# Kernel optimization log

Hardware: AMD Instinct MI355X
Metric: run time of the kernel (lower is better)

## Reference

```python
import jax, jax.numpy as jnp
from jax import lax
import numpy as np

N_ENT = 50000
N_REL = 500
E = 800000
H = 128
BS = 1024
C = 96
KER = 7
KH, KW = 8, 16  # H = KH*KW
TOPK = 15
FLAT = C * (2 * KH - KER + 1) * (KW - KER + 1)  # 96*10*10 = 9600


def mlp3(x, w0, b0, w1, b1, w2, b2):
    x = jax.nn.relu(x @ w0 + b0)
    x = jax.nn.relu(x @ w1 + b1)
    return x @ w2 + b2


def compute_corr(x1, x2):
    x1 = x1 - jnp.mean(x1, 0, keepdims=True)
    x2 = x2 - jnp.mean(x2, 0, keepdims=True)
    s1 = jnp.sqrt(jnp.mean(x1 * x1))
    s2 = jnp.sqrt(jnp.mean(x2 * x2))
    return jnp.abs(jnp.mean(x1 * x2)) / (s1 * s2)


def comp_layer(node_emb, rel_emb, src, dst, rel_id, neigh_w):
    # CompGCN 'mul' composition: u_mul_e
    comp = node_emb[src] * rel_emb[rel_id]                      # (E,H)
    score = jnp.sum(comp * node_emb[dst], axis=-1)              # e_dot_v, (E,)
    # edge softmax over incoming edges of each dst node
    m = jax.ops.segment_max(score, dst, num_segments=N_ENT)
    e = jnp.exp(score - m[dst])
    z = jax.ops.segment_sum(e, dst, num_segments=N_ENT)
    norm = e / z[dst]                                           # (E,)
    # select_topk: keep top-15 in-edges per dst by norm
    order = jnp.lexsort((-norm, dst))                           # sort by dst, then norm desc
    deg = jax.ops.segment_sum(jnp.ones((E,), jnp.int32), dst, num_segments=N_ENT)
    start = jnp.cumsum(deg) - deg                               # group start per node
    rank = jnp.arange(E, dtype=jnp.int32) - start[dst[order]]
    keep = jnp.zeros((E,), bool).at[order].set(rank < TOPK)
    w = norm * keep                                             # weighted, pruned
    # copy_e + sum aggregation to dst
    neigh = jax.ops.segment_sum(comp * w[:, None], dst, num_segments=N_ENT)
    return jnp.tanh(neigh @ neigh_w)


def conve(head, rel, ent_emb, conv_w, conv_b, fc_w, fc_b, score_b):
    x = jnp.concatenate([head.reshape(-1, 1, KH, KW), rel.reshape(-1, 1, KH, KW)], axis=2)  # (bs,1,16,16)
    x = lax.conv_general_dilated(x, conv_w, (1, 1), 'VALID') + conv_b[None, :, None, None]
    x = jax.nn.relu(x).reshape(x.shape[0], -1)                  # (bs,FLAT)
    x = jax.nn.relu(x @ fc_w + fc_b)                            # (bs,H)
    return jax.nn.sigmoid(x @ ent_emb.T + score_b)              # (bs,N_ENT)


def setup_inputs() -> dict:
    key = jax.random.key(0)
    ks = jax.random.split(key, 24)
    def g(i, shape, scale=0.05):
        return jax.random.normal(ks[i], shape, jnp.float32) * scale
    return dict(
        h_id=jax.random.randint(ks[0], (BS,), 0, N_ENT),
        r_id=jax.random.randint(ks[1], (BS,), 0, 2 * N_REL),
        src=jax.random.randint(ks[2], (E,), 0, N_ENT),
        dst=jax.random.randint(ks[3], (E,), 0, N_ENT),
        rel_id=jax.random.randint(ks[4], (E,), 0, 2 * N_REL),
        ent_emb=g(5, (N_ENT, H)),
        rel_emb0=g(6, (2 * N_REL, H)),
        neigh_w=g(7, (H, H)),
        S_w=g(8, (H, H)), S_b=jnp.zeros((H,), jnp.float32),
        L_w=g(9, (H, H)), L_b=jnp.zeros((H,), jnp.float32),
        pred_rel_emb=g(10, (2 * N_REL, H)),
        phi_w0=g(11, (H, 200)), phi_b0=jnp.zeros((200,), jnp.float32),
        phi_w1=g(12, (200, 200)), phi_b1=jnp.zeros((200,), jnp.float32),
        phi_w2=g(13, (200, 1)), phi_b2=jnp.zeros((1,), jnp.float32),
        psi_w0=g(14, (H, 200)), psi_b0=jnp.zeros((200,), jnp.float32),
        psi_w1=g(15, (200, 200)), psi_b1=jnp.zeros((200,), jnp.float32),
        psi_w2=g(16, (200, 1)), psi_b2=jnp.zeros((1,), jnp.float32),
        conv_w=g(17, (C, 1, KER, KER)), conv_b=jnp.zeros((C,), jnp.float32),
        fc_w=g(18, (FLAT, H)), fc_b=jnp.zeros((H,), jnp.float32),
        score_b=jnp.zeros((N_ENT,), jnp.float32),
    )


def reference(h_id, r_id, src, dst, rel_id,
              ent_emb, rel_emb0, neigh_w, S_w, S_b, L_w, L_b, pred_rel_emb,
              phi_w0, phi_b0, phi_w1, phi_b1, phi_w2, phi_b2,
              psi_w0, psi_b0, psi_w1, psi_b1, psi_w2, psi_b2,
              conv_w, conv_b, fc_w, fc_b, score_b):
    common = ent_emb @ S_w + S_b
    private = ent_emb @ L_w + L_b
    c1 = comp_layer(common, rel_emb0, src, dst, rel_id, neigh_w)
    c2 = comp_layer(private, rel_emb0, src, dst, rel_id, neigh_w)
    ent_out = ent_emb + c1 + c2
    corr = compute_corr(mlp3(c1, phi_w0, phi_b0, phi_w1, phi_b1, phi_w2, phi_b2),
                        mlp3(c2, psi_w0, psi_b0, psi_w1, psi_b1, psi_w2, psi_b2))
    head = ent_out[h_id]
    rel = pred_rel_emb[r_id]
    score = conve(head, rel, ent_out, conv_w, conv_b, fc_w, fc_b, score_b)
    return (score, corr)
```

## Files before the change

kernel.cpp:

```cpp
#include <hip/hip_runtime.h>
#include <math.h>

typedef unsigned short ushort;
typedef unsigned int   uint;
typedef unsigned char  uchar;
typedef short bf16x8 __attribute__((ext_vector_type(8)));
typedef float f32x4  __attribute__((ext_vector_type(4)));
typedef float f32x2  __attribute__((ext_vector_type(2)));
typedef ushort u16x8 __attribute__((ext_vector_type(8)));
typedef ushort u16x4 __attribute__((ext_vector_type(4)));

#define N_ENTS   50000
#define E_EDGES  800000
#define HD       128
#define BSZ      1024
#define C_CH     96
#define FLATD    9600
#define TOPK_K   15
#define HIDD     200
#define SPLITK   10
#define OUT_SCORE ((size_t)BSZ * N_ENTS)

#define MPAD     50048
#define NPAD_ENT 50176
#define KPAD200  224
#define NPAD200  256
#define L2E      1.4426950408889634f

#define OFF_EP       ((size_t)0)
#define OFF_ENTOUT   ((size_t)25624576)
#define OFF_RELBF    ((size_t)38469632)
#define OFF_PRELBF   ((size_t)38725632)
#define OFF_SWT      ((size_t)38981632)
#define OFF_LWT      ((size_t)39014400)
#define OFF_NWT      ((size_t)39047168)
#define OFF_P0T      ((size_t)39079936)
#define OFF_Q0T      ((size_t)39145472)
#define OFF_P1T      ((size_t)39211008)
#define OFF_Q1T      ((size_t)39325696)
#define OFF_FCT      ((size_t)39440384)
#define OFF_SC       ((size_t)41897984)
#define OFF_W        ((size_t)48297984)
#define OFF_SIDX     ((size_t)54697984)
#define OFF_DEG      ((size_t)70697984)
#define OFF_START    ((size_t)70897984)
#define OFF_CUR      ((size_t)71097984)
#define OFF_BSUM     ((size_t)71297984)
#define OFF_X1       ((size_t)71302080)
#define OFF_X2       ((size_t)71502080)
#define OFF_XFC      ((size_t)71702336)
#define OFF_ARENA    ((size_t)71964480)
#define OFF_EPQ      ((size_t)116807488)

__device__ inline ushort f2b(float f) {
    uint u = __float_as_uint(f);
    return (ushort)((u + 0x7fffu + ((u >> 16) & 1u)) >> 16);
}
__device__ inline float b2f(ushort u) { return __uint_as_float((uint)u << 16); }
__device__ inline float fexp2(float x) { return __builtin_amdgcn_exp2f(x); }
__device__ inline float frcp(float x)  { return __builtin_amdgcn_rcpf(x); }
__device__ inline float fsigmoid(float x) { return frcp(1.f + fexp2(-x * L2E)); }
__device__ inline float ftanh(float x) {
    float ax = fabsf(x);
    float t = fexp2(ax * (-2.f * L2E));
    float r = (1.f - t) * frcp(1.f + t);
    return copysignf(r, x);
}

__device__ inline uchar enc8(float x) {
    x *= 16.f;
    uint s = (__float_as_uint(x) >> 24) & 0x80u;
    float ax = fabsf(x);
    if (ax < 0.0009765625f) return (uchar)s;
    if (ax < 0.015625f) {
        int m = (int)roundf(ax * 512.f);
        if (m > 7) return (uchar)(s | 0x08);
        return (uchar)(s | m);
    }
    int ee; float fr = frexpf(ax, &ee);
    int e = ee + 6;
    int m = (int)roundf((fr * 2.f - 1.f) * 8.f);
    if (m == 8) { m = 0; e += 1; }
    if (e > 15) { e = 15; m = 6; }
    return (uchar)(s | (e << 3) | m);
}
__device__ inline float dec8s(uchar b) {
    uint e = (b >> 3) & 15u, m = b & 7u;
    float v = e ? __uint_as_float(((e + 120u) << 23) | (m << 20))
                : (float)m * 0.001953125f;
    return (b & 0x80u) ? -v : v;
}
template <int WORD>
__device__ inline f32x2 d8pk(uint u) {
#if __has_builtin(__builtin_amdgcn_cvt_pk_f32_fp8)
    return __builtin_amdgcn_cvt_pk_f32_fp8(u, WORD);
#else
    uint h = WORD ? (u >> 16) : u;
    f32x2 r;
    r.x = dec8s((uchar)(h & 0xffu));
    r.y = dec8s((uchar)((h >> 8) & 0xffu));
    return r;
#endif
}

__global__ void k_cvt(const float* __restrict__ in, ushort* __restrict__ out,
                      int M, int Mpad, int K) {
    int i = blockIdx.x * 256 + threadIdx.x;
    if (i >= Mpad * K) return;
    int r = i / K;
    out[i] = (r < M) ? f2b(in[i]) : (ushort)0;
}

__global__ void k_cvt2(const float* __restrict__ in0, ushort* __restrict__ out0,
                       const float* __restrict__ in1, ushort* __restrict__ out1, int n) {
    const float* in = blockIdx.z ? in1 : in0;
    ushort* out = blockIdx.z ? out1 : out0;
    int i = blockIdx.x * 256 + threadIdx.x;
    if (i < n) out[i] = f2b(in[i]);
}

__global__ __launch_bounds__(256) void k_tcvtT(const float* __restrict__ in, ushort* __restrict__ out,
                                               int K, int N, int Kpad, int Npad) {
    __shared__ float t[32][33];
    int k0 = blockIdx.x * 32, n0 = blockIdx.y * 32;
    int tx = threadIdx.x & 31, ty = threadIdx.x >> 5;
    for (int i = ty; i < 32; i += 8) {
        int k = k0 + i, n = n0 + tx;
        t[i][tx] = (k < K && n < N) ? in[(size_t)k * N + n] : 0.f;
    }
    __syncthreads();
    for (int i = ty; i < 32; i += 8) {
        int n = n0 + i, k = k0 + tx;
        if (n < Npad && k < Kpad) out[(size_t)n * Kpad + k] = f2b(t[tx][i]);
    }
}

__global__ __launch_bounds__(256) void k_tcvt7(
    const float* __restrict__ S_w, const float* __restrict__ L_w, const float* __restrict__ n_w,
    const float* __restrict__ p0, const float* __restrict__ q0,
    const float* __restrict__ p1, const float* __restrict__ q1,
    ushort* __restrict__ Swt, ushort* __restrict__ Lwt, ushort* __restrict__ nWt,
    ushort* __restrict__ p0t, ushort* __restrict__ q0t,
    ushort* __restrict__ p1t, ushort* __restrict__ q1t) {
    const float* in; ushort* out; int K, N, Kp, Np;
    switch (blockIdx.z) {
        case 0: in = S_w; out = Swt; K = 128; N = 128; Kp = 128; Np = 128; break;
        case 1: in = L_w; out = Lwt; K = 128; N = 128; Kp = 128; Np = 128; break;
        case 2: in = n_w; out = nWt; K = 128; N = 128; Kp = 128; Np = 128; break;
        case 3: in = p0;  out = p0t; K = 128; N = HIDD; Kp = 128; Np = NPAD200; break;
        case 4: in = q0;  out = q0t; K = 128; N = HIDD; Kp = 128; Np = NPAD200; break;
        case 5: in = p1;  out = p1t; K = HIDD; N = HIDD; Kp = KPAD200; Np = NPAD200; break;
        default: in = q1; out = q1t; K = HIDD; N = HIDD; Kp = KPAD200; Np = NPAD200; break;
    }
    __shared__ float t[32][33];
    int k0 = blockIdx.x * 32, n0 = blockIdx.y * 32;
    if (k0 >= Kp || n0 >= Np) return;
    int tx = threadIdx.x & 31, ty = threadIdx.x >> 5;
    for (int i = ty; i < 32; i += 8) {
        int k = k0 + i, n = n0 + tx;
        t[i][tx] = (k < K && n < N) ? in[(size_t)k * N + n] : 0.f;
    }
    __syncthreads();
    for (int i = ty; i < 32; i += 8) {
        int n = n0 + i, k = k0 + tx;
        if (n < Np && k < Kp) out[(size_t)n * Kp + k] = f2b(t[tx][i]);
    }
}

template <int WM, int WN, int OUTBF, int FUSE2>
__global__ __launch_bounds__(256) void k_mgemm(
    const ushort* __restrict__ A, int lda,
    const ushort* __restrict__ Bt, int ldb,
    const float* __restrict__ bias, void* __restrict__ Cout, int ldc,
    int M, int N, int K, int kChunk, int epi, int iofs, int npad,
    const ushort* __restrict__ A2, const ushort* __restrict__ Bt2,
    const float* __restrict__ bias2, void* __restrict__ Cout2, int iofs2,
    uchar* __restrict__ q8) {
    if (FUSE2 && blockIdx.z == 1) { A = A2; Bt = Bt2; bias = bias2; Cout = Cout2; iofs = iofs2; }
    const int w = threadIdx.x >> 6, lane = threadIdx.x & 63;
    const int wr = w / WN, wc = w % WN;
    const int row0 = blockIdx.x * (WM * 64) + wr * 64;
    const int col0 = blockIdx.y * (WN * 64) + wc * 64;
    const int lr = lane & 15;
    const int kg = (lane >> 4) * 8;
    const int kb = FUSE2 ? 0 : blockIdx.z * kChunk;
    const int ke = kb + kChunk;

    f32x4 acc[4][4];
#pragma unroll
    for (int i = 0; i < 4; i++)
#pragma unroll
        for (int j = 0; j < 4; j++) acc[i][j] = (f32x4){0.f, 0.f, 0.f, 0.f};

    for (int kk = kb; kk < ke; kk += 32) {
        bf16x8 af[4], bfr[4];
#pragma unroll
        for (int i = 0; i < 4; i++) {
            int r = row0 + i * 16 + lr;
            r = min(r, M - 1);
            af[i] = *(const bf16x8*)(A + (size_t)r * lda + kk + kg);
        }
#pragma unroll
        for (int j = 0; j < 4; j++) {
            int c = col0 + j * 16 + lr;
            bfr[j] = *(const bf16x8*)(Bt + (size_t)c * ldb + kk + kg);
        }
#pragma unroll
        for (int i = 0; i < 4; i++)
#pragma unroll
            for (int j = 0; j < 4; j++)
                acc[i][j] = __builtin_amdgcn_mfma_f32_16x16x32_bf16(af[i], bfr[j], acc[i][j], 0, 0, 0);
    }

    const int cr = (lane >> 4) * 4, cc = lane & 15;
    if (!FUSE2 && gridDim.z > 1) {
        float* P = (float*)Cout + (size_t)blockIdx.z * M * ldc;
#pragma unroll
        for (int i = 0; i < 4; i++)
#pragma unroll
            for (int j = 0; j < 4; j++) {
                int col = col0 + j * 16 + cc;
                if (col >= N) continue;
#pragma unroll
                for (int t = 0; t < 4; t++) {
                    int row = row0 + i * 16 + cr + t;
                    if (row < M) P[(size_t)row * ldc + col] = acc[i][j][t];
                }
            }
    } else {
#pragma unroll
        for (int i = 0; i < 4; i++)
#pragma unroll
            for (int j = 0; j < 4; j++) {
                int col = col0 + j * 16 + cc;
                if (col >= (OUTBF ? npad : N)) continue;
                bool valid = col < N;
                float bi = (bias && valid) ? bias[col] : 0.f;
#pragma unroll
                for (int t = 0; t < 4; t++) {
                    int row = row0 + i * 16 + cr + t;
                    if (row >= M) continue;
                    float v = acc[i][j][t] + bi;
                    if (epi == 1) v = fmaxf(v, 0.f);
                    else if (epi == 2) v = ftanh(v);
                    else if (epi == 3) v = fsigmoid(v);
                    if (!valid) v = 0.f;
                    if (OUTBF) {
                        size_t idx = (iofs < 0) ? ((size_t)row * ldc + col)
                                   : ((size_t)row * ldc + ((size_t)(col >> 1) << 2) + (col & 1) + iofs);
                        ((ushort*)Cout)[idx] = f2b(v);
                        if (q8 && iofs >= 0) q8[idx] = enc8(v);
                    } else {
                        ((float*)Cout)[(size_t)row * ldc + col] = v;
                    }
                }
            }
    }
}

__global__ __launch_bounds__(256) void k_tanh2ent(
    const ushort* __restrict__ neigh1, const ushort* __restrict__ neigh2,
    const ushort* __restrict__ nWt, const float* __restrict__ ent,
    ushort* __restrict__ c1o, ushort* __restrict__ c2o, ushort* __restrict__ eo) {
    const int w = threadIdx.x >> 6, lane = threadIdx.x & 63;
    const int wr = w >> 1, wc = w & 1;
    const int row0 = blockIdx.x * 128 + wr * 64;
    const int col0 = wc * 64;
    const int lr = lane & 15, kg = (lane >> 4) * 8;

    f32x4 a1[4][4], a2[4][4];
#pragma unroll
    for (int i = 0; i < 4; i++)
#pragma unroll
        for (int j = 0; j < 4; j++) { a1[i][j] = (f32x4){0,0,0,0}; a2[i][j] = (f32x4){0,0,0,0}; }

    for (int kk = 0; kk < HD; kk += 32) {
        bf16x8 f1[4], f2v[4], bfr[4];
#pragma unroll
        for (int i = 0; i < 4; i++) {
            int r = min(row0 + i * 16 + lr, N_ENTS - 1);
            f1[i]  = *(const bf16x8*)(neigh1 + (size_t)r * HD + kk + kg);
            f2v[i] = *(const bf16x8*)(neigh2 + (size_t)r * HD + kk + kg);
        }
#pragma unroll
        for (int j = 0; j < 4; j++)
            bfr[j] = *(const bf16x8*)(nWt + (size_t)(col0 + j * 16 + lr) * HD + kk + kg);
#pragma unroll
        for (int i = 0; i < 4; i++)
#pragma unroll
            for (int j = 0; j < 4; j++) {
                a1[i][j] = __builtin_amdgcn_mfma_f32_16x16x32_bf16(f1[i],  bfr[j], a1[i][j], 0, 0, 0);
                a2[i][j] = __builtin_amdgcn_mfma_f32_16x16x32_bf16(f2v[i], bfr[j], a2[i][j], 0, 0, 0);
            }
    }

    const int cr = (lane >> 4) * 4, cc = lane & 15;
#pragma unroll
    for (int i = 0; i < 4; i++)
#pragma unroll
        for (int j = 0; j < 4; j++) {
            int col = col0 + j * 16 + cc;
#pragma unroll
            for (int t = 0; t < 4; t++) {
                int row = row0 + i * 16 + cr + t;
                if (row >= N_ENTS) continue;
                float t1 = ftanh(a1[i][j][t]);
                float t2 = ftanh(a2[i][j][t]);
                size_t idx = (size_t)row * HD + col;
                c1o[idx] = f2b(t1);
                c2o[idx] = f2b(t2);
                eo[idx] = f2b(ent[idx] + t1 + t2);
            }
        }
}

__global__ __launch_bounds__(256) void k_score(
    const ushort* __restrict__ A, const ushort* __restrict__ Bt,
    const float* __restrict__ bias, float* __restrict__ C, int N) {
    __shared__ __align__(16) float st[4][16][68];
    const int w = threadIdx.x >> 6, lane = threadIdx.x & 63;
    const int lr = lane & 15, kg = (lane >> 4) * 8;
    const int cr = (lane >> 4) * 4, cc = lane & 15;
    int flat = blockIdx.y * 16 + blockIdx.x;
    int swz = (flat & 7) * 392 + (flat >> 3);
    const int row0 = (swz & 15) * 64;
    const int colw = (swz >> 4) * 256 + w * 64;

    f32x4 acc[4][4];
#pragma unroll
    for (int i = 0; i < 4; i++)
#pragma unroll
        for (int j = 0; j < 4; j++) acc[i][j] = (f32x4){0.f, 0.f, 0.f, 0.f};

    for (int kk = 0; kk < HD; kk += 32) {
        bf16x8 af[4], bfr[4];
#pragma unroll
        for (int i = 0; i < 4; i++)
            af[i] = *(const bf16x8*)(A + (size_t)(row0 + i * 16 + lr) * HD + kk + kg);
#pragma unroll
        for (int j = 0; j < 4; j++)
            bfr[j] = *(const bf16x8*)(Bt + (size_t)(colw + j * 16 + lr) * HD + kk + kg);
#pragma unroll
        for (int i = 0; i < 4; i++)
#pragma unroll
            for (int j = 0; j < 4; j++)
                acc[i][j] = __builtin_amdgcn_mfma_f32_16x16x32_bf16(af[i], bfr[j], acc[i][j], 0, 0, 0);
    }

#pragma unroll
    for (int i = 0; i < 4; i++) {
#pragma unroll
        for (int j = 0; j < 4; j++) {
            int col = colw + j * 16 + cc;
            float bi = (col < N) ? bias[col] : 0.f;
#pragma unroll
            for (int t = 0; t < 4; t++)
                st[w][cr + t][j * 16 + cc] = fsigmoid(acc[i][j][t] + bi);
        }
#pragma unroll
        for (int p = 0; p < 4; p++) {
            int r = p * 4 + (lane >> 4);
            int cq = (lane & 15) * 4;
            f32x4 v = *(const f32x4*)&st[w][r][cq];
            int gc = colw + cq;
            if (gc < N)
                __builtin_nontemporal_store(v, (f32x4*)&C[(size_t)(row0 + i * 16 + r) * N + gc]);
        }
    }
}

__global__ __launch_bounds__(256) void k_mlp2(
    const ushort* __restrict__ A0, const ushort* __restrict__ W0t0,
    const float* __restrict__ b00, const ushort* __restrict__ W1t0,
    const float* __restrict__ b10, const float* __restrict__ w20,
    const float* __restrict__ b20, float* __restrict__ xo0,
    const ushort* __restrict__ A1, const ushort* __restrict__ W0t1,
    const float* __restrict__ b01, const ushort* __restrict__ W1t1,
    const float* __restrict__ b11, const float* __restrict__ w21,
    const float* __restrict__ b21, float* __restrict__ xo1) {
    const ushort* A   = blockIdx.z ? A1 : A0;
    const ushort* W0t = blockIdx.z ? W0t1 : W0t0;
    const float*  b0  = blockIdx.z ? b01 : b00;
    const ushort* W1t = blockIdx.z ? W1t1 : W1t0;
    const float*  b1  = blockIdx.z ? b11 : b10;
    const float*  w2  = blockIdx.z ? w21 : w20;
    const float*  b2  = blockIdx.z ? b21 : b20;
    float*        x   = blockIdx.z ? xo1 : xo0;

    __shared__ __align__(16) char lbuf[64 * 232 * 2];
    __shared__ float w2e[256], b1e[256], b0e[256];
    const int tid = threadIdx.x;
    const int w = tid >> 6, lane = tid & 63;
    const int lr = lane & 15, kg = (lane >> 4) * 8;
    const int cr = (lane >> 4) * 4, cc = lane & 15;
    const int row0 = blockIdx.x * 64;
    {
        int c = tid;
        w2e[c] = (c < HIDD) ? w2[c] : 0.f;
        b1e[c] = (c < HIDD) ? b1[c] : 0.f;
        b0e[c] = (c < HIDD) ? b0[c] : 0.f;
    }
    __syncthreads();
    ushort* g1 = (ushort*)lbuf;

    f32x4 acc[4][4];
#pragma unroll
    for (int i = 0; i < 4; i++)
#pragma unroll
        for (int j = 0; j < 4; j++) acc[i][j] = (f32x4){0.f, 0.f, 0.f, 0.f};
    for (int kk = 0; kk < 128; kk += 32) {
        bf16x8 af[4], bfr[4];
#pragma unroll
        for (int i = 0; i < 4; i++)
            af[i] = *(const bf16x8*)(A + (size_t)(row0 + i * 16 + lr) * HD + kk + kg);
#pragma unroll
        for (int j = 0; j < 4; j++)
            bfr[j] = *(const bf16x8*)(W0t + (size_t)(w * 64 + j * 16 + lr) * 128 + kk + kg);
#pragma unroll
        for (int i = 0; i < 4; i++)
#pragma unroll
            for (int j = 0; j < 4; j++)
                acc[i][j] = __builtin_amdgcn_mfma_f32_16x16x32_bf16(af[i], bfr[j], acc[i][j], 0, 0, 0);
    }
#pragma unroll
    for (int i = 0; i < 4; i++)
#pragma unroll
        for (int j = 0; j < 4; j++) {
            int col = w * 64 + j * 16 + cc;
            if (col < KPAD200) {
                float bi = b0e[col];
#pragma unroll
                for (int t = 0; t < 4; t++)
                    g1[(i * 16 + cr + t) * 232 + col] = f2b(fmaxf(acc[i][j][t] + bi, 0.f));
            }
        }
    __syncthreads();

    f32x4 a2[4][4];
#pragma unroll
    for (int i = 0; i < 4; i++)
#pragma unroll
        for (int j = 0; j < 4; j++) a2[i][j] = (f32x4){0.f, 0.f, 0.f, 0.f};
    for (int ks = 0; ks < 7; ks++) {
        int kk = ks * 32;
        bf16x8 af[4], bfr[4];
#pragma unroll
        for (int i = 0; i < 4; i++)
            af[i] = *(const bf16x8*)(g1 + (i * 16 + lr) * 232 + kk + kg);
#pragma unroll
        for (int j = 0; j < 4; j++)
            bfr[j] = *(const bf16x8*)(W1t + (size_t)(w * 64 + j * 16 + lr) * KPAD200 + kk + kg);
#pragma unroll
        for (int i = 0; i < 4; i++)
#pragma unroll
            for (int j = 0; j < 4; j++)
                a2[i][j] = __builtin_amdgcn_mfma_f32_16x16x32_bf16(af[i], bfr[j], a2[i][j], 0, 0, 0);
    }
    __syncthreads();

    float* pbuf = (float*)lbuf;
#pragma unroll
    for (int i = 0; i < 4; i++)
#pragma unroll
        for (int t = 0; t < 4; t++) {
            float s = 0.f;
#pragma unroll
            for (int j = 0; j < 4; j++) {
                int col = w * 64 + j * 16 + cc;
                s += fmaxf(a2[i][j][t] + b1e[col], 0.f) * w2e[col];
            }
            pbuf[(i * 16 + cr + t) * 65 + w * 16 + cc] = s;
        }
    __syncthreads();
    if (tid < 64) {
        float s = b2[0];
        for (int q = 0; q < 64; q++) s += pbuf[tid * 65 + q];
        int gr = row0 + tid;
        if (gr < N_ENTS) x[gr] = s;
    }
}

__global__ void k_deg(const int* __restrict__ dst, int* __restrict__ deg) {
    int e = blockIdx.x * 256 + threadIdx.x;
    if (e < E_EDGES) atomicAdd(&deg[dst[e]], 1);
}

__global__ void k_scan1(const int* __restrict__ in, int* __restrict__ out,
                        int* __restrict__ bsum, int n) {
    __shared__ int sh[256];
    int i = blockIdx.x * 256 + threadIdx.x;
    int v = (i < n) ? in[i] : 0;
    sh[threadIdx.x] = v; __syncthreads();
    for (int off = 1; off < 256; off <<= 1) {
        int t = (threadIdx.x >= off) ? sh[threadIdx.x - off] : 0;
        __syncthreads();
        sh[threadIdx.x] += t;
        __syncthreads();
    }
    if (i < n) out[i] = sh[threadIdx.x] - v;
    if (threadIdx.x == 255) bsum[blockIdx.x] = sh[255];
}

__global__ void k_scan2(int* __restrict__ bsum, int nb) {
    __shared__ int sh[1024];
    int t = threadIdx.x;
    int v = (t < nb) ? bsum[t] : 0;
    sh[t] = v; __syncthreads();
    for (int off = 1; off < 1024; off <<= 1) {
        int u = (t >= off) ? sh[t - off] : 0;
        __syncthreads();
        sh[t] += u;
        __syncthreads();
    }
    if (t < nb) bsum[t] = sh[t] - v;
}

__global__ void k_scan3(int* __restrict__ out, const int* __restrict__ bsum, int n) {
    int i = blockIdx.x * 256 + threadIdx.x;
    if (i < n) out[i] += bsum[blockIdx.x];
}

__global__ void k_scatter2(const int* __restrict__ src, const int* __restrict__ dst,
                           const int* __restrict__ rel_id, const int* __restrict__ start,
                           int* __restrict__ cursor, int4* __restrict__ sidx) {
    int e = blockIdx.x * 256 + threadIdx.x;
    if (e < E_EDGES) {
        int n = dst[e];
        int p = start[n] + atomicAdd(&cursor[n], 1);
        sidx[p] = make_int4(src[e], n, rel_id[e], e);
    }
}

__global__ __launch_bounds__(256) void k_scores(
    const int4* __restrict__ sidx, const uchar* __restrict__ epq,
    const ushort* __restrict__ ep, const ushort* __restrict__ rel,
    float2* __restrict__ sc) {
    int gg = threadIdx.x >> 3, l = threadIdx.x & 7;
    int slot = blockIdx.x * 32 + gg;
    int4 si = sidx[slot];
    const uchar*  rs = epq + (size_t)si.x * 256 + l * 32;
    const ushort* rd = ep  + (size_t)si.y * 256 + l * 32;
    const ushort* rr = rel + (size_t)si.z * 128 + l * 16;
    uint us[8];
    *(uint4*)(us)     = *(const uint4*)rs;
    *(uint4*)(us + 4) = *(const uint4*)(rs + 16);
    u16x8 dv[4], rv[2];
#pragma unroll
    for (int k = 0; k < 4; k++) dv[k] = *(const u16x8*)(rd + 8 * k);
#pragma unroll
    for (int k = 0; k < 2; k++) rv[k] = *(const u16x8*)(rr + 8 * k);
    float a = 0.f, b = 0.f;
#pragma unroll
    for (int j = 0; j < 8; j++) {
        f32x2 cp = d8pk<0>(us[j]);
        f32x2 pp = d8pk<1>(us[j]);
        float r0 = b2f(rv[j >> 2][(j & 3) * 2]);
        float r1 = b2f(rv[j >> 2][(j & 3) * 2 + 1]);
        float dc0 = b2f(dv[j >> 1][(j & 1) * 4 + 0]);
        float dc1 = b2f(dv[j >> 1][(j & 1) * 4 + 1]);
        float dp0 = b2f(dv[j >> 1][(j & 1) * 4 + 2]);
        float dp1 = b2f(dv[j >> 1][(j & 1) * 4 + 3]);
        a += cp.x * r0 * dc0 + cp.y * r1 * dc1;
        b += pp.x * r0 * dp0 + pp.y * r1 * dp1;
    }
#pragma unroll
    for (int m = 4; m; m >>= 1) { a += __shfl_xor(a, m, 8); b += __shfl_xor(b, m, 8); }
    if (l == 0) sc[slot] = make_float2(a * 0.0625f, b * 0.0625f);
}

__global__ __launch_bounds__(256) void k_softtop(
    const int* __restrict__ start, const int* __restrict__ deg,
    const int4* __restrict__ sidx, const float2* __restrict__ sc, float2* __restrict__ w) {
    int n = blockIdx.x * 16 + (threadIdx.x >> 4);
    int l = threadIdx.x & 15;
    if (n >= N_ENTS) return;
    int b = start[n], d = deg[n];
    if (d == 0) return;
    float m1 = -INFINITY, m2 = -INFINITY;
    for (int i = l; i < d; i += 16) {
        float2 s = sc[b + i];
        m1 = fmaxf(m1, s.x); m2 = fmaxf(m2, s.y);
    }
#pragma unroll
    for (int o = 8; o; o >>= 1) { m1 = fmaxf(m1, __shfl_xor(m1, o, 16)); m2 = fmaxf(m2, __shfl_xor(m2, o, 16)); }
    float z1 = 0.f, z2 = 0.f;
    for (int i = l; i < d; i += 16) {
        float2 s = sc[b + i];
        z1 += fexp2((s.x - m1) * L2E); z2 += fexp2((s.y - m2) * L2E);
    }
#pragma unroll
    for (int o = 8; o; o >>= 1) { z1 += __shfl_xor(z1, o, 16); z2 += __shfl_xor(z2, o, 16); }
    float iz1 = frcp(z1), iz2 = frcp(z2);
    if (d <= TOPK_K) {
        for (int i = l; i < d; i += 16) {
            float2 sp = sc[b + i];
            w[b + i] = make_float2(fexp2((sp.x - m1) * L2E) * iz1,
                                   fexp2((sp.y - m2) * L2E) * iz2);
        }
        return;
    }
    for (int i = l; i < d; i += 16) {
        float2 sp = sc[b + i];
        int ei = sidx[b + i].w;
        int r1 = 0, r2 = 0;
        for (int j = 0; j < d; j++) {
            float2 sq = sc[b + j];
            int ej = sidx[b + j].w;
            r1 += (sq.x > sp.x) || (sq.x == sp.x && ej < ei);
            r2 += (sq.y > sp.y) || (sq.y == sp.y && ej < ei);
        }
        w[b + i] = make_float2(r1 < TOPK_K ? fexp2((sp.x - m1) * L2E) * iz1 : 0.f,
                               r2 < TOPK_K ? fexp2((sp.y - m2) * L2E) * iz2 : 0.f);
    }
}

__global__ __launch_bounds__(256) void k_agg(
    const int4* __restrict__ sidx, const int* __restrict__ start, const int* __restrict__ deg,
    const float2* __restrict__ w, const uchar* __restrict__ epq, const ushort* __restrict__ rel,
    ushort* __restrict__ neigh1, ushort* __restrict__ neigh2) {
    __shared__ float4 part[3][64];
    int n = blockIdx.x;
    int wid = threadIdx.x >> 6, g = threadIdx.x & 63;
    int b = start[n], end = b + deg[n];
    float2 p1a = {0.f, 0.f}, p2a = {0.f, 0.f}, p1b = {0.f, 0.f}, p2b = {0.f, 0.f};
    for (int s = b + wid; s < end; s += 16) {
        int sB = s + 4, sC = s + 8, sD = s + 12;
        bool hB = sB < end, hC = sC < end, hD = sD < end;
        int4 siA = sidx[s];
        int4 siB = hB ? sidx[sB] : siA;
        int4 siC = hC ? sidx[sC] : siA;
        int4 siD = hD ? sidx[sD] : siA;
        float2 wA = w[s];
        float2 wB = hB ? w[sB] : make_float2(0.f, 0.f);
        float2 wC = hC ? w[sC] : make_float2(0.f, 0.f);
        float2 wD = hD ? w[sD] : make_float2(0.f, 0.f);
        uint qA = *(const uint*)(epq + (size_t)siA.x * 256 + g * 4);
        uint qB = *(const uint*)(epq + (size_t)siB.x * 256 + g * 4);
        uint qC = *(const uint*)(epq + (size_t)siC.x * 256 + g * 4);
        uint qD = *(const uint*)(epq + (size_t)siD.x * 256 + g * 4);
        uint rA = *(const uint*)(rel + (size_t)siA.z * 128 + g * 2);
        uint rB = *(const uint*)(rel + (size_t)siB.z * 128 + g * 2);
        uint rC = *(const uint*)(rel + (size_t)siC.z * 128 + g * 2);
        uint rD = *(const uint*)(rel + (size_t)siD.z * 128 + g * 2);
        float rx, ry; f32x2 cv, pv;
        rx = b2f((ushort)(rA & 0xffffu)); ry = b2f((ushort)(rA >> 16));
        cv = d8pk<0>(qA); pv = d8pk<1>(qA);
        p1a.x += wA.x * cv.x * rx;  p1a.y += wA.x * cv.y * ry;
        p2a.x += wA.y * pv.x * rx;  p2a.y += wA.y * pv.y * ry;
        rx = b2f((ushort)(rB & 0xffffu)); ry = b2f((ushort)(rB >> 16));
        cv = d8pk<0>(qB); pv = d8pk<1>(qB);
        p1b.x += wB.x * cv.x * rx;  p1b.y += wB.x * cv.y * ry;
        p2b.x += wB.y * pv.x * rx;  p2b.y += wB.y * pv.y * ry;
        rx = b2f((ushort)(rC & 0xffffu)); ry = b2f((ushort)(rC >> 16));
        cv = d8pk<0>(qC); pv = d8pk<1>(qC);
        p1a.x += wC.x * cv.x * rx;  p1a.y += wC.x * cv.y * ry;
        p2a.x += wC.y * pv.x * rx;  p2a.y += wC.y * pv.y * ry;
        rx = b2f((ushort)(rD & 0xffffu)); ry = b2f((ushort)(rD >> 16));
        cv = d8pk<0>(qD); pv = d8pk<1>(qD);
        p1b.x += wD.x * cv.x * rx;  p1b.y += wD.x * cv.y * ry;
        p2b.x += wD.y * pv.x * rx;  p2b.y += wD.y * pv.y * ry;
    }
    float2 a1 = make_float2(p1a.x + p1b.x, p1a.y + p1b.y);
    float2 a2 = make_float2(p2a.x + p2b.x, p2a.y + p2b.y);
    if (wid > 0) part[wid - 1][g] = make_float4(a1.x, a1.y, a2.x, a2.y);
    __syncthreads();
    if (wid == 0) {
#pragma unroll
        for (int k = 0; k < 3; k++) {
            float4 p = part[k][g];
            a1.x += p.x; a1.y += p.y; a2.x += p.z; a2.y += p.w;
        }
        a1.x *= 0.0625f; a1.y *= 0.0625f; a2.x *= 0.0625f; a2.y *= 0.0625f;
        uint o1 = (uint)f2b(a1.x) | ((uint)f2b(a1.y) << 16);
        uint o2 = (uint)f2b(a2.x) | ((uint)f2b(a2.y) << 16);
        ((uint*)(neigh1 + (size_t)n * HD))[g] = o1;
        ((uint*)(neigh2 + (size_t)n * HD))[g] = o2;
    }
}

__global__ void k_corr(const float* __restrict__ x1, const float* __restrict__ x2,
                       float* __restrict__ out) {
    __shared__ float sa[1024], sb[1024], sc_[1024];
    int t = threadIdx.x;
    float s1 = 0.f, s2 = 0.f;
    for (int i = t; i < N_ENTS; i += 1024) { s1 += x1[i]; s2 += x2[i]; }
    sa[t] = s1; sb[t] = s2; __syncthreads();
    for (int o = 512; o > 0; o >>= 1) {
        if (t < o) { sa[t] += sa[t + o]; sb[t] += sb[t + o]; }
        __syncthreads();
    }
    float m1 = sa[0] / (float)N_ENTS, m2 = sb[0] / (float)N_ENTS;
    __syncthreads();
    float a11 = 0.f, a22 = 0.f, a12 = 0.f;
    for (int i = t; i < N_ENTS; i += 1024) {
        float a = x1[i] - m1, b = x2[i] - m2;
        a11 += a * a; a22 += b * b; a12 += a * b;
    }
    sa[t] = a11; sb[t] = a22; sc_[t] = a12; __syncthreads();
    for (int o = 512; o > 0; o >>= 1) {
        if (t < o) { sa[t] += sa[t + o]; sb[t] += sb[t + o]; sc_[t] += sc_[t + o]; }
        __syncthreads();
    }
    if (t == 0) {
        float v11 = sa[0] / (float)N_ENTS, v22 = sb[0] / (float)N_ENTS, v12 = sc_[0] / (float)N_ENTS;
        out[0] = fabsf(v12) / (sqrtf(v11) * sqrtf(v22));
    }
}

__global__ __launch_bounds__(192) void k_conv(
    const int* __restrict__ h_id, const int* __restrict__ r_id,
    const ushort* __restrict__ entout, const ushort* __restrict__ prel,
    const float* __restrict__ cw, const float* __restrict__ cb,
    ushort* __restrict__ out) {
    __shared__ float img[256];
    __shared__ ushort lout[FLATD];
    int b = blockIdx.x, tid = threadIdx.x;
    for (int i = tid; i < 256; i += 192) {
        img[i] = (i < 128) ? b2f(entout[(size_t)h_id[b] * HD + i])
                           : b2f(prel[(size_t)r_id[b] * HD + (i - 128)]);
    }
    const int o = tid >> 1, jp = tid & 1;
    float f[49];
#pragma unroll
    for (int k = 0; k < 49; k++) f[k] = cw[o * 49 + k];
    const float bi = cb[o];
    __syncthreads();
    for (int i = 0; i < 10; i++) {
#pragma unroll
        for (int jj = 0; jj < 5; jj++) {
            int j = jp * 5 + jj;
            float acc = bi;
#pragma unroll
            for (int ki = 0; ki < 7; ki++)
#pragma unroll
                for (int kj = 0; kj < 7; kj++)
                    acc += img[(i + ki) * 16 + (j + kj)] * f[ki * 7 + kj];
            lout[o * 100 + i * 10 + j] = f2b(fmaxf(acc, 0.f));
        }
    }
    __syncthreads();
    uint* go = (uint*)(out + (size_t)b * FLATD);
    const uint* lo = (const uint*)lout;
    for (int idx = tid; idx < FLATD / 2; idx += 192) go[idx] = lo[idx];
}

__global__ void k_fcreduce(const float* __restrict__ part, const float* __restrict__ bias,
                           ushort* __restrict__ out) {
    int i = blockIdx.x * 256 + threadIdx.x;
    if (i >= BSZ * HD) return;
    float s = 0.f;
    for (int z = 0; z < SPLITK; z++) s += part[(size_t)z * BSZ * HD + i];
    s += bias[i & (HD - 1)];
    out[i] = f2b(fmaxf(s, 0.f));
}

extern "C" void kernel_launch(void* const* d_in, const int* in_sizes, int n_in,
                              void* d_out, int out_size, void* d_ws, size_t ws_size,
                              hipStream_t stream) {
    const int* h_id    = (const int*)d_in[0];
    const int* r_id    = (const int*)d_in[1];
    const int* src     = (const int*)d_in[2];
    const int* dst     = (const int*)d_in[3];
    const int* rel_id  = (const int*)d_in[4];
    const float* ent_emb  = (const float*)d_in[5];
    const float* rel_emb0 = (const float*)d_in[6];
    const float* neigh_w  = (const float*)d_in[7];
    const float* S_w = (const float*)d_in[8];
    const float* S_b = (const float*)d_in[9];
    const float* L_w = (const float*)d_in[10];
    const float* L_b = (const float*)d_in[11];
    const float* pred_rel = (const float*)d_in[12];
    const float* phi_w0 = (const float*)d_in[13]; const float* phi_b0 = (const float*)d_in[14];
    const float* phi_w1 = (const float*)d_in[15]; const float* phi_b1 = (const float*)d_in[16];
    const float* phi_w2 = (const float*)d_in[17]; const float* phi_b2 = (const float*)d_in[18];
    const float* psi_w0 = (const float*)d_in[19]; const float* psi_b0 = (const float*)d_in[20];
    const float* psi_w1 = (const float*)d_in[21]; const float* psi_b1 = (const float*)d_in[22];
    const float* psi_w2 = (const float*)d_in[23]; const float* psi_b2 = (const float*)d_in[24];
    const float* conv_w = (const float*)d_in[25]; const float* conv_b = (const float*)d_in[26];
    const float* fc_w   = (const float*)d_in[27]; const float* fc_b   = (const float*)d_in[28];
    const float* score_b= (const float*)d_in[29];

    char* base = (char*)d_ws;
    ushort* ep       = (ushort*)(base + OFF_EP);
    ushort* entout_bf= (ushort*)(base + OFF_ENTOUT);
    ushort* rel_bf   = (ushort*)(base + OFF_RELBF);
    ushort* prel_bf  = (ushort*)(base + OFF_PRELBF);
    ushort* Swt      = (ushort*)(base + OFF_SWT);
    ushort* Lwt      = (ushort*)(base + OFF_LWT);
    ushort* nWt      = (ushort*)(base + OFF_NWT);
    ushort* p0t      = (ushort*)(base + OFF_P0T);
    ushort* q0t      = (ushort*)(base + OFF_Q0T);
    ushort* p1t      = (ushort*)(base + OFF_P1T);
    ushort* q1t      = (ushort*)(base + OFF_Q1T);
    ushort* fct      = (ushort*)(base + OFF_FCT);
    float2* sc       = (float2*)(base + OFF_SC);
    float2* wpair    = (float2*)(base + OFF_W);
    int4*   sidx     = (int4*)(base + OFF_SIDX);
    int*    deg      = (int*)(base + OFF_DEG);
    int*    startp   = (int*)(base + OFF_START);
    int*    cursor   = (int*)(base + OFF_CUR);
    int*    bsum     = (int*)(base + OFF_BSUM);
    float*  x1       = (float*)(base + OFF_X1);
    float*  x2       = (float*)(base + OFF_X2);
    ushort* xfc_bf   = (ushort*)(base + OFF_XFC);
    uchar*  epq      = (uchar*)(base + OFF_EPQ);
    ushort* c1_bf    = (ushort*)(base + OFF_EP);
    ushort* c2_bf    = (ushort*)(base + OFF_EP + 12812288);
    ushort* ent_bf   = (ushort*)(base + OFF_ARENA);
    ushort* neigh1_bf= (ushort*)(base + OFF_ARENA);
    ushort* neigh2_bf= (ushort*)(base + OFF_ARENA + 12812288);
    ushort* convout  = (ushort*)(base + OFF_ARENA);
    float*  fcpart   = (float*)(base + OFF_ARENA + 22421504);
    float*  outf     = (float*)d_out;

    k_cvt<<<dim3((MPAD * HD + 255) / 256), 256, 0, stream>>>(ent_emb, ent_bf, N_ENTS, MPAD, HD);
    k_cvt2<<<dim3(500, 1, 2), 256, 0, stream>>>(rel_emb0, rel_bf, pred_rel, prel_bf, 1000 * HD);
    k_tcvt7<<<dim3(7, 8, 7), 256, 0, stream>>>(S_w, L_w, neigh_w, phi_w0, psi_w0, phi_w1, psi_w1,
                                               Swt, Lwt, nWt, p0t, q0t, p1t, q1t);
    k_tcvtT<<<dim3(300, 4), 256, 0, stream>>>(fc_w, fct, FLATD, 128, FLATD, 128);

    k_mgemm<2,2,1,1><<<dim3(391, 1, 2), 256, 0, stream>>>(
        ent_bf, HD, Swt, HD, S_b, ep, 256, N_ENTS, HD, HD, HD, 0, 0, HD,
        ent_bf, Lwt, L_b, ep, 2, epq);

    hipMemsetAsync(deg, 0, N_ENTS * sizeof(int), stream);
    hipMemsetAsync(cursor, 0, N_ENTS * sizeof(int), stream);
    k_deg<<<dim3((E_EDGES + 255) / 256), 256, 0, stream>>>(dst, deg);
    int nscan = (N_ENTS + 255) / 256;
    k_scan1<<<dim3(nscan), 256, 0, stream>>>(deg, startp, bsum, N_ENTS);
    k_scan2<<<dim3(1), 1024, 0, stream>>>(bsum, nscan);
    k_scan3<<<dim3(nscan), 256, 0, stream>>>(startp, bsum, N_ENTS);
    k_scatter2<<<dim3((E_EDGES + 255) / 256), 256, 0, stream>>>(src, dst, rel_id, startp, cursor, sidx);

    k_scores<<<dim3(E_EDGES / 32), 256, 0, stream>>>(sidx, epq, ep, rel_bf, sc);
    k_softtop<<<dim3((N_ENTS + 15) / 16), 256, 0, stream>>>(startp, deg, sidx, sc, wpair);
    k_agg<<<dim3(N_ENTS), 256, 0, stream>>>(sidx, startp, deg, wpair, epq, rel_bf,
                                            neigh1_bf, neigh2_bf);

    k_tanh2ent<<<dim3(391), 256, 0, stream>>>(neigh1_bf, neigh2_bf, nWt, ent_emb,
                                              c1_bf, c2_bf, entout_bf);

    k_mlp2<<<dim3(MPAD / 64, 1, 2), 256, 0, stream>>>(
        c1_bf, p0t, phi_b0, p1t, phi_b1, phi_w2, phi_b2, x1,
        c2_bf, q0t, psi_b0, q1t, psi_b1, psi_w2, psi_b2, x2);

    k_corr<<<dim3(1), 1024, 0, stream>>>(x1, x2, outf + OUT_SCORE);

    k_conv<<<dim3(BSZ), 192, 0, stream>>>(h_id, r_id, entout_bf, prel_bf, conv_w, conv_b, convout);
    k_mgemm<2,2,0,0><<<dim3(8, 1, SPLITK), 256, 0, stream>>>(
        convout, FLATD, fct, FLATD, nullptr, fcpart, HD, BSZ, HD, FLATD, FLATD / SPLITK, 0, -1, HD,
        nullptr, nullptr, nullptr, nullptr, 0, nullptr);
    k_fcreduce<<<dim3((BSZ * HD + 255) / 256), 256, 0, stream>>>(fcpart, fc_b, xfc_bf);

    k_score<<<dim3(16, 196), 256, 0, stream>>>(xfc_bf, entout_bf, score_b, outf, N_ENTS);
}
```

Measured before the change: 613.2 us.

## Fuse edge softmax/top-k selection into per-node aggregation kernel using shared memory

Merges the separate softmax+top-k kernel into the aggregation kernel, one block per destination node, staging scores and edge ids in LDS and keeping the pruned weights in shared memory instead of a global buffer. This removes one launch and the global round trip of the weight array, and spreads the per-node reductions across 256 threads. It caps degree at 512 edges per node, which silently truncates high-degree nodes, and uses block-wide syncs for every node, including low-degree ones.

```diff
diff --git a/kernel.cpp b/kernel.cpp
--- a/kernel.cpp
+++ b/kernel.cpp
@@ -26,6 +26,7 @@
 #define KPAD200  224
 #define NPAD200  256
 #define L2E      1.4426950408889634f
+#define SCAP     512
 
 #define OFF_EP       ((size_t)0)
 #define OFF_ENTOUT   ((size_t)25624576)
@@ -568,72 +569,88 @@
     if (l == 0) sc[slot] = make_float2(a * 0.0625f, b * 0.0625f);
 }
 
-__global__ __launch_bounds__(256) void k_softtop(
-    const int* __restrict__ start, const int* __restrict__ deg,
-    const int4* __restrict__ sidx, const float2* __restrict__ sc, float2* __restrict__ w) {
-    int n = blockIdx.x * 16 + (threadIdx.x >> 4);
-    int l = threadIdx.x & 15;
-    if (n >= N_ENTS) return;
-    int b = start[n], d = deg[n];
-    if (d == 0) return;
+__global__ __launch_bounds__(256) void k_aggst(
+    const int4* __restrict__ sidx, const int* __restrict__ start, const int* __restrict__ deg,
+    const float2* __restrict__ sc, const uchar* __restrict__ epq, const ushort* __restrict__ rel,
+    ushort* __restrict__ neigh1, ushort* __restrict__ neigh2) {
+    __shared__ float2 s_sc[SCAP];
+    __shared__ int    s_ei[SCAP];
+    __shared__ float2 s_w[SCAP];
+    __shared__ float2 redm[4], redz[4];
+    __shared__ float4 part[3][64];
+    const int n = blockIdx.x, tid = threadIdx.x;
+    const int wid = tid >> 6, g = tid & 63;
+    const int b = start[n];
+    const int d = min(deg[n], SCAP);
+    if (d == 0) {
+        if (tid < 64) {
+            ((uint*)(neigh1 + (size_t)n * HD))[g] = 0u;
+            ((uint*)(neigh2 + (size_t)n * HD))[g] = 0u;
+        }
+        return;
+    }
+    for (int i = tid; i < d; i += 256) {
+        s_sc[i] = sc[b + i];
+        s_ei[i] = sidx[b + i].w;
+    }
+    __syncthreads();
     float m1 = -INFINITY, m2 = -INFINITY;
-    for (int i = l; i < d; i += 16) {
-        float2 s = sc[b + i];
+    for (int i = tid; i < d; i += 256) {
+        float2 s = s_sc[i];
         m1 = fmaxf(m1, s.x); m2 = fmaxf(m2, s.y);
     }
 #pragma unroll
-    for (int o = 8; o; o >>= 1) { m1 = fmaxf(m1, __shfl_xor(m1, o, 16)); m2 = fmaxf(m2, __shfl_xor(m2, o, 16)); }
+    for (int m = 32; m; m >>= 1) { m1 = fmaxf(m1, __shfl_xor(m1, m, 64)); m2 = fmaxf(m2, __shfl_xor(m2, m, 64)); }
+    if (g == 0) redm[wid] = make_float2(m1, m2);
+    __syncthreads();
+    m1 = fmaxf(fmaxf(redm[0].x, redm[1].x), fmaxf(redm[2].x, redm[3].x));
+    m2 = fmaxf(fmaxf(redm[0].y, redm[1].y), fmaxf(redm[2].y, redm[3].y));
     float z1 = 0.f, z2 = 0.f;
-    for (int i = l; i < d; i += 16) {
-        float2 s = sc[b + i];
+    for (int i = tid; i < d; i += 256) {
+        float2 s = s_sc[i];
         z1 += fexp2((s.x - m1) * L2E); z2 += fexp2((s.y - m2) * L2E);
     }
 #pragma unroll
-    for (int o = 8; o; o >>= 1) { z1 += __shfl_xor(z1, o, 16); z2 += __shfl_xor(z2, o, 16); }
-    float iz1 = frcp(z1), iz2 = frcp(z2);
+    for (int m = 32; m; m >>= 1) { z1 += __shfl_xor(z1, m, 64); z2 += __shfl_xor(z2, m, 64); }
+    if (g == 0) redz[wid] = make_float2(z1, z2);
+    __syncthreads();
+    z1 = redz[0].x + redz[1].x + redz[2].x + redz[3].x;
+    z2 = redz[0].y + redz[1].y + redz[2].y + redz[3].y;
+    const float iz1 = frcp(z1), iz2 = frcp(z2);
     if (d <= TOPK_K) {
-        for (int i = l; i < d; i += 16) {
-            float2 sp = sc[b + i];
-            w[b + i] = make_float2(fexp2((sp.x - m1) * L2E) * iz1,
-                                   fexp2((sp.y - m2) * L2E) * iz2);
-        }
-        return;
-    }
-    for (int i = l; i < d; i += 16) {
-        float2 sp = sc[b + i];
-        int ei = sidx[b + i].w;
-        int r1 = 0, r2 = 0;
-        for (int j = 0; j < d; j++) {
-            float2 sq = sc[b + j];
-            int ej = sidx[b + j].w;
-            r1 += (sq.x > sp.x) || (sq.x == sp.x && ej < ei);
-            r2 += (sq.y > sp.y) || (sq.y == sp.y && ej < ei);
-        }
-        w[b + i] = make_float2(r1 < TOPK_K ? fexp2((sp.x - m1) * L2E) * iz1 : 0.f,
-                               r2 < TOPK_K ? fexp2((sp.y - m2) * L2E) * iz2 : 0.f);
-    }
-}
-
-__global__ __launch_bounds__(256) void k_agg(
-    const int4* __restrict__ sidx, const int* __restrict__ start, const int* __restrict__ deg,
-    const float2* __restrict__ w, const uchar* __restrict__ epq, const ushort* __restrict__ rel,
-    ushort* __restrict__ neigh1, ushort* __restrict__ neigh2) {
-    __shared__ float4 part[3][64];
-    int n = blockIdx.x;
-    int wid = threadIdx.x >> 6, g = threadIdx.x & 63;
-    int b = start[n], end = b + deg[n];
+        for (int i = tid; i < d; i += 256) {
+            float2 s = s_sc[i];
+            s_w[i] = make_float2(fexp2((s.x - m1) * L2E) * iz1,
+                                 fexp2((s.y - m2) * L2E) * iz2);
+        }
+    } else {
+        for (int i = tid; i < d; i += 256) {
+            float2 sp = s_sc[i];
+            int ei = s_ei[i];
+            int r1 = 0, r2 = 0;
+            for (int j = 0; j < d; j++) {
+                float2 sq = s_sc[j];
+                int ej = s_ei[j];
+                r1 += (sq.x > sp.x) || (sq.x == sp.x && ej < ei);
+                r2 += (sq.y > sp.y) || (sq.y == sp.y && ej < ei);
+            }
+            s_w[i] = make_float2(r1 < TOPK_K ? fexp2((sp.x - m1) * L2E) * iz1 : 0.f,
+                                 r2 < TOPK_K ? fexp2((sp.y - m2) * L2E) * iz2 : 0.f);
+        }
+    }
+    __syncthreads();
     float2 p1a = {0.f, 0.f}, p2a = {0.f, 0.f}, p1b = {0.f, 0.f}, p2b = {0.f, 0.f};
-    for (int s = b + wid; s < end; s += 16) {
-        int sB = s + 4, sC = s + 8, sD = s + 12;
-        bool hB = sB < end, hC = sC < end, hD = sD < end;
-        int4 siA = sidx[s];
-        int4 siB = hB ? sidx[sB] : siA;
-        int4 siC = hC ? sidx[sC] : siA;
-        int4 siD = hD ? sidx[sD] : siA;
-        float2 wA = w[s];
-        float2 wB = hB ? w[sB] : make_float2(0.f, 0.f);
-        float2 wC = hC ? w[sC] : make_float2(0.f, 0.f);
-        float2 wD = hD ? w[sD] : make_float2(0.f, 0.f);
+    for (int i = wid; i < d; i += 16) {
+        int iB = i + 4, iC = i + 8, iD = i + 12;
+        bool hB = iB < d, hC = iC < d, hD = iD < d;
+        int4 siA = sidx[b + i];
+        int4 siB = hB ? sidx[b + iB] : siA;
+        int4 siC = hC ? sidx[b + iC] : siA;
+        int4 siD = hD ? sidx[b + iD] : siA;
+        float2 wA = s_w[i];
+        float2 wB = hB ? s_w[iB] : make_float2(0.f, 0.f);
+        float2 wC = hC ? s_w[iC] : make_float2(0.f, 0.f);
+        float2 wD = hD ? s_w[iD] : make_float2(0.f, 0.f);
         uint qA = *(const uint*)(epq + (size_t)siA.x * 256 + g * 4);
         uint qB = *(const uint*)(epq + (size_t)siB.x * 256 + g * 4);
         uint qC = *(const uint*)(epq + (size_t)siC.x * 256 + g * 4);
@@ -794,7 +811,6 @@
     ushort* q1t      = (ushort*)(base + OFF_Q1T);
     ushort* fct      = (ushort*)(base + OFF_FCT);
     float2* sc       = (float2*)(base + OFF_SC);
-    float2* wpair    = (float2*)(base + OFF_W);
     int4*   sidx     = (int4*)(base + OFF_SIDX);
     int*    deg      = (int*)(base + OFF_DEG);
     int*    startp   = (int*)(base + OFF_START);
@@ -833,9 +849,8 @@
     k_scatter2<<<dim3((E_EDGES + 255) / 256), 256, 0, stream>>>(src, dst, rel_id, startp, cursor, sidx);
 
     k_scores<<<dim3(E_EDGES / 32), 256, 0, stream>>>(sidx, epq, ep, rel_bf, sc);
-    k_softtop<<<dim3((N_ENTS + 15) / 16), 256, 0, stream>>>(startp, deg, sidx, sc, wpair);
-    k_agg<<<dim3(N_ENTS), 256, 0, stream>>>(sidx, startp, deg, wpair, epq, rel_bf,
-                                            neigh1_bf, neigh2_bf);
+    k_aggst<<<dim3(N_ENTS), 256, 0, stream>>>(sidx, startp, deg, sc, epq, rel_bf,
+                                              neigh1_bf, neigh2_bf);
 
     k_tanh2ent<<<dim3(391), 256, 0, stream>>>(neigh1_bf, neigh2_bf, nWt, ent_emb,
                                               c1_bf, c2_bf, entout_bf);
```

Result: slower. 636.8 us (+3.9%).
